# Performance work log

Hardware: AMD Instinct MI355X
Metric: run time of the kernel (lower is better)

Reference implementation:

```python
import jax, jax.numpy as jnp
import numpy as np

PI = np.pi


def _apply_1q(state, gate, wire, n):
    # state: [B, 2**n] complex64; gate: [2,2] (shared) or [B,2,2] (per-sample)
    # PennyLane convention: wire 0 is the most-significant bit of the state index.
    B = state.shape[0]
    left, right = 2 ** wire, 2 ** (n - wire - 1)
    s = state.reshape(B, left, 2, right)
    if gate.ndim == 2:
        s = jnp.einsum('kl,balr->bakr', gate, s)
    else:
        s = jnp.einsum('bkl,balr->bakr', gate, s)
    return s.reshape(B, -1)


def _apply_cz(state, wire, n):
    # CZ on (wire, wire+1): flip sign of |..11..> amplitudes
    B = state.shape[0]
    left, right = 2 ** wire, 2 ** (n - wire - 2)
    s = state.reshape(B, left, 2, 2, right)
    s = s.at[:, :, 1, 1, :].multiply(-1.0)
    return s.reshape(B, -1)


def _ry_batched(theta):
    # theta: [B] -> [B,2,2] complex RY(theta)
    h = 0.5 * theta
    c, s = jnp.cos(h), jnp.sin(h)
    g = jnp.stack([jnp.stack([c, -s], -1), jnp.stack([s, c], -1)], -2)
    return g.astype(jnp.complex64)


def _rot(phi, theta, omega):
    # Rot = RZ(omega) @ RY(theta) @ RZ(phi)
    c, s = jnp.cos(0.5 * theta), jnp.sin(0.5 * theta)
    e_mm = jnp.exp(-0.5j * (phi + omega))
    e_pm = jnp.exp(0.5j * (phi - omega))
    e_mp = jnp.exp(-0.5j * (phi - omega))
    e_pp = jnp.exp(0.5j * (phi + omega))
    g = jnp.stack([jnp.stack([e_mm * c, -e_pm * s]), jnp.stack([e_mp * s, e_pp * c])])
    return g.astype(jnp.complex64)


def _simulate(enc, weights):
    # enc: [B, n_qubits] in [-1,1]; weights: [n_layers, n_qubits, 3]
    n_layers, n, _ = weights.shape
    B = enc.shape[0]
    state = jnp.zeros((B, 2 ** n), jnp.complex64).at[:, 0].set(1.0)
    ry = [_ry_batched(enc[:, i] * PI) for i in range(n)]
    for l in range(n_layers):
        for i in range(n):
            state = _apply_1q(state, ry[i], i, n)
        for i in range(n):
            state = _apply_1q(state, _rot(weights[l, i, 0], weights[l, i, 1], weights[l, i, 2]), i, n)
        for i in range(n - 1):
            state = _apply_cz(state, i, n)
    for i in range(n):
        state = _apply_1q(state, ry[i], i, n)
    probs = state.real ** 2 + state.imag ** 2  # [B, 2**n]
    # <Z_i> = sum_k probs[k] * (-1)^bit_i(k), wire 0 = MSB
    bits = (jnp.arange(2 ** n)[None, :] >> (n - 1 - jnp.arange(n))[:, None]) & 1
    signs = (1 - 2 * bits).astype(probs.dtype)  # [n, 2**n]
    return probs @ signs.T  # [B, n]


def setup_inputs() -> dict:
    B, D, NQ, NL, NA = 32768, 16, 8, 4, 4
    key = jax.random.key(0)
    ks = jax.random.split(key, 6)

    def lin(k, o, i):
        b = 1.0 / np.sqrt(i)
        k1, k2 = jax.random.split(k)
        return (jax.random.uniform(k1, (o, i), jnp.float32, -b, b),
                jax.random.uniform(k2, (o,), jnp.float32, -b, b))

    enc_w1, enc_b1 = lin(ks[1], 8, D)
    enc_w2, enc_b2 = lin(ks[2], NQ, 8)
    dec_w1, dec_b1 = lin(ks[3], 8, NQ)
    dec_w2, dec_b2 = lin(ks[4], NA, 8)
    q_weights = jax.random.uniform(ks[5], (NL, NQ, 3), jnp.float32, 0.0, 2.0 * PI)
    x = jax.random.normal(ks[0], (B, D), jnp.float32)
    return {"x": x, "enc_w1": enc_w1, "enc_b1": enc_b1, "enc_w2": enc_w2, "enc_b2": enc_b2,
            "q_weights": q_weights, "dec_w1": dec_w1, "dec_b1": dec_b1, "dec_w2": dec_w2, "dec_b2": dec_b2}


def reference(x, enc_w1, enc_b1, enc_w2, enc_b2, q_weights, dec_w1, dec_b1, dec_w2, dec_b2):
    h = jax.nn.relu(x @ enc_w1.T + enc_b1)
    enc = jnp.tanh(h @ enc_w2.T + enc_b2)          # [B, n_qubits]
    q = _simulate(enc, q_weights)                  # [B, n_qubits] PauliZ expvals
    h2 = jax.nn.relu(q @ dec_w1.T + dec_b1)
    return h2 @ dec_w2.T + dec_b2                  # [B, n_actions]
```

## Files before the change

### kernel.cpp

```cpp
#include <hip/hip_runtime.h>
#include <math.h>


#define PI_F 3.14159265358979323846f

typedef float v2f __attribute__((ext_vector_type(2)));

struct C2 { float re, im; };
__device__ __forceinline__ C2 cmul(C2 a, C2 b) {
    C2 r;
    r.re = fmaf(a.re, b.re, -a.im * b.im);
    r.im = fmaf(a.re, b.im,  a.im * b.re);
    return r;
}
__device__ __forceinline__ float fxor(float x, int m) {
    return __int_as_float(__float_as_int(x) ^ m);
}

__device__ __forceinline__ v2f pk_mul(v2f a, v2f b) {
    v2f d; asm("v_pk_mul_f32 %0, %1, %2" : "=v"(d) : "v"(a), "v"(b)); return d;
}
__device__ __forceinline__ v2f pk_mul_neg(v2f a, v2f b) {
    v2f d; asm("v_pk_mul_f32 %0, %1, %2 neg_lo:[1,0] neg_hi:[1,0]"
               : "=v"(d) : "v"(a), "v"(b)); return d;
}
__device__ __forceinline__ v2f pk_fma(v2f a, v2f b, v2f c) {
    v2f d; asm("v_pk_fma_f32 %0, %1, %2, %3" : "=v"(d) : "v"(a), "v"(b), "v"(c)); return d;
}
__device__ __forceinline__ v2f pk_fma_nn(v2f a, v2f b, v2f c) {
    v2f d; asm("v_pk_fma_f32 %0, %1, %2, %3 neg_lo:[1,0,0] neg_hi:[1,0,0]"
               : "=v"(d) : "v"(a), "v"(b), "v"(c)); return d;
}
__device__ __forceinline__ v2f pk_fma_swl(v2f a, v2f b, v2f c) {
    v2f d; asm("v_pk_fma_f32 %0, %1, %2, %3 op_sel:[0,1,0] op_sel_hi:[1,0,1] neg_lo:[1,0,0]"
               : "=v"(d) : "v"(a), "v"(b), "v"(c)); return d;
}
__device__ __forceinline__ v2f pk_fma_swh(v2f a, v2f b, v2f c) {
    v2f d; asm("v_pk_fma_f32 %0, %1, %2, %3 op_sel:[0,1,0] op_sel_hi:[1,0,1] neg_hi:[1,0,0]"
               : "=v"(d) : "v"(a), "v"(b), "v"(c)); return d;
}

template<int CTRL>
__device__ __forceinline__ float dppf(float x) {
    int xi = __float_as_int(x);
    int r = __builtin_amdgcn_update_dpp(xi, xi, CTRL, 0xF, 0xF, false);
    return __int_as_float(r);
}
template<int M>
__device__ __forceinline__ float lxor(float x) {
    if constexpr (M == 1)      return dppf<0xB1>(x);
    else if constexpr (M == 2) return dppf<0x4E>(x);
    else if constexpr (M == 4) return __int_as_float(
        __builtin_amdgcn_ds_swizzle(__float_as_int(x), 0x101F));
    else                       return dppf<0x128>(x);
}

__device__ __forceinline__ void load_G2(const float* __restrict__ c_lds, int g,
                                        float cc, float ss,
                                        float& ar, float& ai, float& br, float& bi) {
    const float4 c0 = *(const float4*)(c_lds + 4 * g);
    ar = fmaf(c0.x, cc, -c0.z * ss);
    ai = fmaf(c0.y, cc,  c0.w * ss);
    br = fmaf(c0.z, cc,  c0.x * ss);
    bi = fmaf(c0.w, cc, -c0.y * ss);
}

template<int M>
__device__ __forceinline__ void su2_cross(v2f cSr, v2f cSi, v2f cOr, v2f cOi,
                                          v2f z[16]) {
#pragma unroll
    for (int t = 0; t < 16; t++) {
        v2f p;
        p.x = lxor<M>(z[t].x);
        p.y = lxor<M>(z[t].y);
        v2f n = pk_mul(cSr, z[t]);
        n = pk_fma_swl(cSi, z[t], n);
        n = pk_fma   (cOr, p, n);
        n = pk_fma_swl(cOi, p, n);
        z[t] = n;
    }
}

template<int ST>
__device__ __forceinline__ void su2_inlane(v2f arr, v2f aii, v2f brr, v2f bii,
                                           v2f z[16]) {
#pragma unroll
    for (int t = 0; t < 16; t++) {
        if ((t & ST) == 0) {
            const int u = t + ST;
            v2f x = z[t], y = z[u];
            v2f nx = pk_mul(arr, x);
            nx = pk_fma_swl(aii, x, nx);
            nx = pk_fma_nn (brr, y, nx);
            nx = pk_fma_swl(bii, y, nx);
            v2f ny = pk_mul(brr, x);
            ny = pk_fma_swl(bii, x, ny);
            ny = pk_fma   (arr, y, ny);
            ny = pk_fma_swh(aii, y, ny);
            z[t] = nx; z[u] = ny;
        }
    }
}

template<int M>
__device__ __forceinline__ void ry_cross(v2f cc, v2f cO, v2f z[16]) {
#pragma unroll
    for (int t = 0; t < 16; t++) {
        v2f p;
        p.x = lxor<M>(z[t].x);
        p.y = lxor<M>(z[t].y);
        z[t] = pk_fma(cO, p, pk_mul(cc, z[t]));
    }
}
template<int ST>
__device__ __forceinline__ void ry_inlane(v2f cc, v2f ss, v2f z[16]) {
#pragma unroll
    for (int t = 0; t < 16; t++) {
        if ((t & ST) == 0) {
            const int u = t + ST;
            v2f x = z[t], y = z[u];
            z[t] = pk_fma_nn(ss, y, pk_mul(cc, x));
            z[u] = pk_fma   (cc, y, pk_mul(ss, x));
        }
    }
}

__device__ __constant__ const bool CZNEG[16] =
    { false,false,false,true,  false,false,true,false,
      false,false,false,true,  true, true, false,true };

__global__ __launch_bounds__(256) void qdqn_kernel(
    const float* __restrict__ x,
    const float* __restrict__ ew1, const float* __restrict__ eb1,
    const float* __restrict__ ew2, const float* __restrict__ eb2,
    const float* __restrict__ qw,
    const float* __restrict__ dw1, const float* __restrict__ db1,
    const float* __restrict__ dw2, const float* __restrict__ db2,
    float* __restrict__ out, int B, int NL) {
    __shared__ __align__(16) float c_lds[32 * 4];

    const int tid = threadIdx.x;
    const int n_gates = NL * 8;

    if (tid < n_gates) {
        const int g = tid;
        float phi = qw[3 * g + 0], th = qw[3 * g + 1], om = qw[3 * g + 2];
        float c = __cosf(0.5f * th), s = __sinf(0.5f * th);
        float A = 0.5f * (phi + om), Bb = 0.5f * (phi - om);
        float* o = c_lds + 4 * g;
        o[0] =  __cosf(A) * c;  o[1] = -__sinf(A) * c;
        o[2] =  __cosf(Bb) * s; o[3] = -__sinf(Bb) * s;
    }
    __syncthreads();

    const int lane = tid & 63;
    const int L = lane & 15;
    int s = blockIdx.x * 16 + (tid >> 4);
    if (s >= B) s = B - 1;

    float xv[16];
    const float4* xp = (const float4*)(x + s * 16);
#pragma unroll
    for (int i = 0; i < 4; i++) {
        float4 v = xp[i];
        xv[4*i] = v.x; xv[4*i+1] = v.y; xv[4*i+2] = v.z; xv[4*i+3] = v.w;
    }
    float hbuf[8];
#pragma unroll
    for (int j = 0; j < 8; j++) {
        float a = eb1[j];
#pragma unroll
        for (int i = 0; i < 16; i++) a = fmaf(ew1[j * 16 + i], xv[i], a);
        hbuf[j] = fmaxf(a, 0.0f);
    }
    float cq[8], sq[8];
#pragma unroll
    for (int q = 0; q < 8; q++) {
        float a = eb2[q];
#pragma unroll
        for (int j = 0; j < 8; j++) a = fmaf(ew2[q * 8 + j], hbuf[j], a);
        float e = 1.0f - __fdividef(2.0f, __expf(2.0f * a) + 1.0f);
        float ang = e * (0.5f * PI_F);
        cq[q] = __cosf(ang);
        sq[q] = __sinf(ang);
    }

    int hiM[4], loM[4];
#pragma unroll
    for (int q = 0; q < 4; q++) {
        int hi = (L >> (3 - q)) & 1;
        hiM[q] = hi << 31;
        loM[q] = hiM[q] ^ 0x80000000;
    }

    const int L0 = L & 1, L1b = (L >> 1) & 1, L2b = (L >> 2) & 1, L3b = (L >> 3) & 1;
    const int cnt = (L3b & L2b) + (L2b & L1b) + (L1b & L0);
    const float mL = (cnt & 1) ? -1.0f : 1.0f;
    const float mH = L0 ? -mL : mL;
    const v2f mL2 = (v2f){mL, mL}, mH2 = (v2f){mH, mH};

    v2f z[16];
    {
        C2 P; P.re = 1.0f; P.im = 0.0f;
        C2 F[4][2];
#pragma unroll
        for (int q = 0; q < 8; q++) {
            float ar, ai, br, bi;
            load_G2(c_lds, q, cq[q], sq[q], ar, ai, br, bi);
            if (q < 4) {
                const bool hi = (L >> (3 - q)) & 1;
                C2 f; f.re = hi ? br : ar; f.im = hi ? bi : ai;
                P = cmul(P, f);
            } else {
                F[q-4][0].re = ar; F[q-4][0].im = ai;
                F[q-4][1].re = br; F[q-4][1].im = bi;
            }
        }
        C2 A0 = cmul(P, F[0][0]), A1 = cmul(P, F[0][1]);
        C2 Bv[4];
        Bv[0] = cmul(A0, F[1][0]); Bv[1] = cmul(A0, F[1][1]);
        Bv[2] = cmul(A1, F[1][0]); Bv[3] = cmul(A1, F[1][1]);
        C2 Cv[8];
#pragma unroll
        for (int i = 0; i < 8; i++) Cv[i] = cmul(Bv[i >> 1], F[2][i & 1]);
#pragma unroll
        for (int t = 0; t < 16; t++) {
            C2 v = cmul(Cv[t >> 1], F[3][t & 1]);
            float m = (t < 8) ? mL : mH;
            m = CZNEG[t] ? -m : m;
            z[t].x = v.re * m;
            z[t].y = v.im * m;
        }
    }

    for (int l = 1; l < NL; l++) {
        const int g0 = l * 8;
        float ar, ai, br, bi;
        load_G2(c_lds, g0+0, cq[0], sq[0], ar, ai, br, bi);
        su2_cross<8>((v2f){ar,ar}, (v2f){fxor(ai,hiM[0]),fxor(ai,hiM[0])},
                     (v2f){fxor(br,loM[0]),fxor(br,loM[0])}, (v2f){bi,bi}, z);
        load_G2(c_lds, g0+1, cq[1], sq[1], ar, ai, br, bi);
        su2_cross<4>((v2f){ar,ar}, (v2f){fxor(ai,hiM[1]),fxor(ai,hiM[1])},
                     (v2f){fxor(br,loM[1]),fxor(br,loM[1])}, (v2f){bi,bi}, z);
        load_G2(c_lds, g0+2, cq[2], sq[2], ar, ai, br, bi);
        su2_cross<2>((v2f){ar,ar}, (v2f){fxor(ai,hiM[2]),fxor(ai,hiM[2])},
                     (v2f){fxor(br,loM[2]),fxor(br,loM[2])}, (v2f){bi,bi}, z);
        load_G2(c_lds, g0+3, cq[3], sq[3], ar, ai, br, bi);
        su2_cross<1>((v2f){ar,ar}, (v2f){fxor(ai,hiM[3]),fxor(ai,hiM[3])},
                     (v2f){fxor(br,loM[3]),fxor(br,loM[3])}, (v2f){bi,bi}, z);
        load_G2(c_lds, g0+4, cq[4], sq[4], ar, ai, br, bi);
        su2_inlane<8>((v2f){ar,ar}, (v2f){ai,ai}, (v2f){br,br}, (v2f){bi,bi}, z);
        load_G2(c_lds, g0+5, cq[5], sq[5], ar, ai, br, bi);
        su2_inlane<4>((v2f){ar,ar}, (v2f){ai,ai}, (v2f){br,br}, (v2f){bi,bi}, z);
        load_G2(c_lds, g0+6, cq[6], sq[6], ar, ai, br, bi);
        su2_inlane<2>((v2f){ar,ar}, (v2f){ai,ai}, (v2f){br,br}, (v2f){bi,bi}, z);
        load_G2(c_lds, g0+7, cq[7], sq[7], ar, ai, br, bi);
        su2_inlane<1>((v2f){ar,ar}, (v2f){ai,ai}, (v2f){br,br}, (v2f){bi,bi}, z);
#pragma unroll
        for (int t = 0; t < 16; t++) {
            v2f m = (t < 8) ? mL2 : mH2;
            z[t] = CZNEG[t] ? pk_mul_neg(m, z[t]) : pk_mul(m, z[t]);
        }
    }

    {
        v2f cc, cO, ss;
        cc=(v2f){cq[0],cq[0]}; cO=(v2f){fxor(sq[0],loM[0]),fxor(sq[0],loM[0])};
        ry_cross<8>(cc, cO, z);
        cc=(v2f){cq[1],cq[1]}; cO=(v2f){fxor(sq[1],loM[1]),fxor(sq[1],loM[1])};
        ry_cross<4>(cc, cO, z);
        cc=(v2f){cq[2],cq[2]}; cO=(v2f){fxor(sq[2],loM[2]),fxor(sq[2],loM[2])};
        ry_cross<2>(cc, cO, z);
        cc=(v2f){cq[3],cq[3]}; cO=(v2f){fxor(sq[3],loM[3]),fxor(sq[3],loM[3])};
        ry_cross<1>(cc, cO, z);
        cc=(v2f){cq[4],cq[4]}; ss=(v2f){sq[4],sq[4]}; ry_inlane<8>(cc, ss, z);
        cc=(v2f){cq[5],cq[5]}; ss=(v2f){sq[5],sq[5]}; ry_inlane<4>(cc, ss, z);
        cc=(v2f){cq[6],cq[6]}; ss=(v2f){sq[6],sq[6]}; ry_inlane<2>(cc, ss, z);
        cc=(v2f){cq[7],cq[7]}; ss=(v2f){sq[7],sq[7]}; ry_inlane<1>(cc, ss, z);
    }

    float p[16];
#pragma unroll
    for (int t = 0; t < 16; t++) p[t] = fmaf(z[t].x, z[t].x, z[t].y * z[t].y);

    float e0 = p[0]+p[1],  e1 = p[2]+p[3],  e2 = p[4]+p[5],  e3 = p[6]+p[7];
    float e4 = p[8]+p[9],  e5 = p[10]+p[11], e6 = p[12]+p[13], e7 = p[14]+p[15];
    float q0 = e0+e1, q1 = e2+e3, q2 = e4+e5, q3 = e6+e7;
    float h0 = q0+q1, h1 = q2+q3;
    float sumP = h0 + h1;

    float zv[8];
#pragma unroll
    for (int w = 0; w < 4; w++)
        zv[w] = ((L >> (3 - w)) & 1) ? -sumP : sumP;
    zv[4] = h0 - h1;
    zv[5] = (q0 - q1) + (q2 - q3);
    zv[6] = (e0 - e1) + (e2 - e3) + (e4 - e5) + (e6 - e7);
    zv[7] = (p[0]-p[1]) + (p[2]-p[3]) + (p[4]-p[5]) + (p[6]-p[7])
          + (p[8]-p[9]) + (p[10]-p[11]) + (p[12]-p[13]) + (p[14]-p[15]);

#pragma unroll
    for (int w = 0; w < 8; w++) zv[w] += lxor<1>(zv[w]);
#pragma unroll
    for (int w = 0; w < 8; w++) zv[w] += lxor<2>(zv[w]);
#pragma unroll
    for (int w = 0; w < 8; w++) zv[w] += lxor<4>(zv[w]);
#pragma unroll
    for (int w = 0; w < 8; w++) zv[w] += lxor<8>(zv[w]);

    float h2[8];
#pragma unroll
    for (int j = 0; j < 8; j++) {
        float a = db1[j];
#pragma unroll
        for (int w = 0; w < 8; w++) a = fmaf(dw1[j * 8 + w], zv[w], a);
        h2[j] = fmaxf(a, 0.0f);
    }
    if (L < 4) {
        float a = db2[L];
#pragma unroll
        for (int j = 0; j < 8; j++) a = fmaf(dw2[L * 8 + j], h2[j], a);
        out[s * 4 + L] = a;
    }
}

extern "C" void kernel_launch(void* const* d_in, const int* in_sizes, int n_in,
                              void* d_out, int out_size, void* d_ws, size_t ws_size,
                              hipStream_t stream) {
    const float* x   = (const float*)d_in[0];
    const float* ew1 = (const float*)d_in[1];
    const float* eb1 = (const float*)d_in[2];
    const float* ew2 = (const float*)d_in[3];
    const float* eb2 = (const float*)d_in[4];
    const float* qw  = (const float*)d_in[5];
    const float* dw1 = (const float*)d_in[6];
    const float* db1 = (const float*)d_in[7];
    const float* dw2 = (const float*)d_in[8];
    const float* db2 = (const float*)d_in[9];
    float* out = (float*)d_out;

    int B = in_sizes[0] / 16;
    int n_gates = in_sizes[5] / 3;
    int NL = n_gates / 8;

    int blocks = (B + 15) / 16;
    qdqn_kernel<<<blocks, 256, 0, stream>>>(x, ew1, eb1, ew2, eb2, qw,
                                            dw1, db1, dw2, db2, out, B, NL);
}
```

Measured before the change: 124.1 us.

## Map each sample to 8 lanes with 32 amplitudes per lane

Each sample's 256-amplitude state now lives on 8 lanes holding 32 amplitudes each, where it used to be 16 lanes holding 16. The top three qubits are handled by cross-lane shuffles and the other five in-lane, and the block shrinks to 128 threads with launch bounds of 128,2. The encoder and decoder MLPs are also split across the 8 lanes, with results exchanged through LDS and wave barriers so each lane no longer computes every hidden unit. This cuts the cross-lane shuffle traffic and redundant MLP work, but the larger per-lane state raises register pressure and gives fewer threads per sample.

```diff
diff --git a/kernel.cpp b/kernel.cpp
--- a/kernel.cpp
+++ b/kernel.cpp
@@ -39,6 +39,10 @@
     v2f d; asm("v_pk_fma_f32 %0, %1, %2, %3 op_sel:[0,1,0] op_sel_hi:[1,0,1] neg_hi:[1,0,0]"
                : "=v"(d) : "v"(a), "v"(b), "v"(c)); return d;
 }
+__device__ __forceinline__ v2f cmulv(v2f z, C2 c) {
+    v2f n = pk_mul((v2f){c.re, c.re}, z);
+    return pk_fma_swl((v2f){c.im, c.im}, z, n);
+}
 
 template<int CTRL>
 __device__ __forceinline__ float dppf(float x) {
@@ -50,9 +54,8 @@
 __device__ __forceinline__ float lxor(float x) {
     if constexpr (M == 1)      return dppf<0xB1>(x);
     else if constexpr (M == 2) return dppf<0x4E>(x);
-    else if constexpr (M == 4) return __int_as_float(
+    else                       return __int_as_float(
         __builtin_amdgcn_ds_swizzle(__float_as_int(x), 0x101F));
-    else                       return dppf<0x128>(x);
 }
 
 __device__ __forceinline__ void load_G2(const float* __restrict__ c_lds, int g,
@@ -67,9 +70,9 @@
 
 template<int M>
 __device__ __forceinline__ void su2_cross(v2f cSr, v2f cSi, v2f cOr, v2f cOi,
-                                          v2f z[16]) {
-#pragma unroll
-    for (int t = 0; t < 16; t++) {
+                                          v2f z[32]) {
+#pragma unroll
+    for (int t = 0; t < 32; t++) {
         v2f p;
         p.x = lxor<M>(z[t].x);
         p.y = lxor<M>(z[t].y);
@@ -83,9 +86,9 @@
 
 template<int ST>
 __device__ __forceinline__ void su2_inlane(v2f arr, v2f aii, v2f brr, v2f bii,
-                                           v2f z[16]) {
-#pragma unroll
-    for (int t = 0; t < 16; t++) {
+                                           v2f z[32]) {
+#pragma unroll
+    for (int t = 0; t < 32; t++) {
         if ((t & ST) == 0) {
             const int u = t + ST;
             v2f x = z[t], y = z[u];
@@ -103,9 +106,9 @@
 }
 
 template<int M>
-__device__ __forceinline__ void ry_cross(v2f cc, v2f cO, v2f z[16]) {
-#pragma unroll
-    for (int t = 0; t < 16; t++) {
+__device__ __forceinline__ void ry_cross(v2f cc, v2f cO, v2f z[32]) {
+#pragma unroll
+    for (int t = 0; t < 32; t++) {
         v2f p;
         p.x = lxor<M>(z[t].x);
         p.y = lxor<M>(z[t].y);
@@ -113,9 +116,9 @@
     }
 }
 template<int ST>
-__device__ __forceinline__ void ry_inlane(v2f cc, v2f ss, v2f z[16]) {
-#pragma unroll
-    for (int t = 0; t < 16; t++) {
+__device__ __forceinline__ void ry_inlane(v2f cc, v2f ss, v2f z[32]) {
+#pragma unroll
+    for (int t = 0; t < 32; t++) {
         if ((t & ST) == 0) {
             const int u = t + ST;
             v2f x = z[t], y = z[u];
@@ -125,11 +128,12 @@
     }
 }
 
-__device__ __constant__ const bool CZNEG[16] =
-    { false,false,false,true,  false,false,true,false,
-      false,false,false,true,  true, true, false,true };
-
-__global__ __launch_bounds__(256) void qdqn_kernel(
+__host__ __device__ constexpr bool czt5(int t) {
+    return ((((t >> 4) & (t >> 3)) ^ ((t >> 3) & (t >> 2)) ^
+             ((t >> 2) & (t >> 1)) ^ ((t >> 1) & t)) & 1) != 0;
+}
+
+__global__ __launch_bounds__(128, 2) void qdqn_kernel(
     const float* __restrict__ x,
     const float* __restrict__ ew1, const float* __restrict__ eb1,
     const float* __restrict__ ew2, const float* __restrict__ eb2,
@@ -138,6 +142,8 @@
     const float* __restrict__ dw2, const float* __restrict__ db2,
     float* __restrict__ out, int B, int NL) {
     __shared__ __align__(16) float c_lds[32 * 4];
+    __shared__ __align__(16) float hx[2][8][8];
+    __shared__ __align__(16) float csx[2][8][16];
 
     const int tid = threadIdx.x;
     const int n_gates = NL * 8;
@@ -153,174 +159,195 @@
     }
     __syncthreads();
 
+    const int wave = tid >> 6;
     const int lane = tid & 63;
-    const int L = lane & 15;
-    int s = blockIdx.x * 16 + (tid >> 4);
+    const int grp = lane >> 3;
+    const int g = lane & 7;
+    int s = blockIdx.x * 16 + wave * 8 + grp;
     if (s >= B) s = B - 1;
 
-    float xv[16];
-    const float4* xp = (const float4*)(x + s * 16);
-#pragma unroll
-    for (int i = 0; i < 4; i++) {
-        float4 v = xp[i];
-        xv[4*i] = v.x; xv[4*i+1] = v.y; xv[4*i+2] = v.z; xv[4*i+3] = v.w;
-    }
-    float hbuf[8];
-#pragma unroll
-    for (int j = 0; j < 8; j++) {
-        float a = eb1[j];
-#pragma unroll
-        for (int i = 0; i < 16; i++) a = fmaf(ew1[j * 16 + i], xv[i], a);
-        hbuf[j] = fmaxf(a, 0.0f);
-    }
     float cq[8], sq[8];
-#pragma unroll
-    for (int q = 0; q < 8; q++) {
-        float a = eb2[q];
-#pragma unroll
-        for (int j = 0; j < 8; j++) a = fmaf(ew2[q * 8 + j], hbuf[j], a);
-        float e = 1.0f - __fdividef(2.0f, __expf(2.0f * a) + 1.0f);
+    {
+        float xv[16];
+        const float4* xp = (const float4*)(x + s * 16);
+#pragma unroll
+        for (int i = 0; i < 4; i++) {
+            float4 v = xp[i];
+            xv[4*i] = v.x; xv[4*i+1] = v.y; xv[4*i+2] = v.z; xv[4*i+3] = v.w;
+        }
+        float a = eb1[g];
+#pragma unroll
+        for (int i = 0; i < 16; i++) a = fmaf(ew1[g * 16 + i], xv[i], a);
+        hx[wave][grp][g] = fmaxf(a, 0.0f);
+        __builtin_amdgcn_wave_barrier();
+        float4 h01 = *(const float4*)&hx[wave][grp][0];
+        float4 h23 = *(const float4*)&hx[wave][grp][4];
+        float b = eb2[g];
+        b = fmaf(ew2[g*8+0], h01.x, b); b = fmaf(ew2[g*8+1], h01.y, b);
+        b = fmaf(ew2[g*8+2], h01.z, b); b = fmaf(ew2[g*8+3], h01.w, b);
+        b = fmaf(ew2[g*8+4], h23.x, b); b = fmaf(ew2[g*8+5], h23.y, b);
+        b = fmaf(ew2[g*8+6], h23.z, b); b = fmaf(ew2[g*8+7], h23.w, b);
+        float e = 1.0f - __fdividef(2.0f, __expf(2.0f * b) + 1.0f);
         float ang = e * (0.5f * PI_F);
-        cq[q] = __cosf(ang);
-        sq[q] = __sinf(ang);
-    }
-
-    int hiM[4], loM[4];
-#pragma unroll
-    for (int q = 0; q < 4; q++) {
-        int hi = (L >> (3 - q)) & 1;
+        float2* cso = (float2*)&csx[wave][grp][2 * g];
+        *cso = make_float2(__cosf(ang), __sinf(ang));
+        __builtin_amdgcn_wave_barrier();
+#pragma unroll
+        for (int k = 0; k < 4; k++) {
+            float4 v = *(const float4*)&csx[wave][grp][4 * k];
+            cq[2*k] = v.x; sq[2*k] = v.y; cq[2*k+1] = v.z; sq[2*k+1] = v.w;
+        }
+    }
+
+    int hiM[3], loM[3];
+#pragma unroll
+    for (int q = 0; q < 3; q++) {
+        int hi = (g >> (2 - q)) & 1;
         hiM[q] = hi << 31;
         loM[q] = hiM[q] ^ 0x80000000;
     }
 
-    const int L0 = L & 1, L1b = (L >> 1) & 1, L2b = (L >> 2) & 1, L3b = (L >> 3) & 1;
-    const int cnt = (L3b & L2b) + (L2b & L1b) + (L1b & L0);
-    const float mL = (cnt & 1) ? -1.0f : 1.0f;
-    const float mH = L0 ? -mL : mL;
-    const v2f mL2 = (v2f){mL, mL}, mH2 = (v2f){mH, mH};
-
-    v2f z[16];
+    const int g0b = g & 1, g1b = (g >> 1) & 1, g2b = (g >> 2) & 1;
+    const float mLo = ((g2b & g1b) ^ (g1b & g0b)) ? -1.0f : 1.0f;
+    const float mHi = g0b ? -mLo : mLo;
+    const v2f mLo2 = (v2f){mLo, mLo}, mHi2 = (v2f){mHi, mHi};
+
+    v2f z[32];
     {
         C2 P; P.re = 1.0f; P.im = 0.0f;
-        C2 F[4][2];
+        C2 A[5], Bc[5];
 #pragma unroll
         for (int q = 0; q < 8; q++) {
             float ar, ai, br, bi;
             load_G2(c_lds, q, cq[q], sq[q], ar, ai, br, bi);
-            if (q < 4) {
-                const bool hi = (L >> (3 - q)) & 1;
+            if (q < 3) {
+                const bool hi = (g >> (2 - q)) & 1;
                 C2 f; f.re = hi ? br : ar; f.im = hi ? bi : ai;
                 P = cmul(P, f);
             } else {
-                F[q-4][0].re = ar; F[q-4][0].im = ai;
-                F[q-4][1].re = br; F[q-4][1].im = bi;
+                A[q-3].re = ar;  A[q-3].im = ai;
+                Bc[q-3].re = br; Bc[q-3].im = bi;
             }
         }
-        C2 A0 = cmul(P, F[0][0]), A1 = cmul(P, F[0][1]);
-        C2 Bv[4];
-        Bv[0] = cmul(A0, F[1][0]); Bv[1] = cmul(A0, F[1][1]);
-        Bv[2] = cmul(A1, F[1][0]); Bv[3] = cmul(A1, F[1][1]);
-        C2 Cv[8];
-#pragma unroll
-        for (int i = 0; i < 8; i++) Cv[i] = cmul(Bv[i >> 1], F[2][i & 1]);
-#pragma unroll
-        for (int t = 0; t < 16; t++) {
-            C2 v = cmul(Cv[t >> 1], F[3][t & 1]);
-            float m = (t < 8) ? mL : mH;
-            m = CZNEG[t] ? -m : m;
-            z[t].x = v.re * m;
-            z[t].y = v.im * m;
+        z[0] = (v2f){P.re, P.im};
+#pragma unroll
+        for (int w = 0; w < 5; w++) {
+            const int n = 1 << w;
+#pragma unroll
+            for (int i = n - 1; i >= 0; i--) {
+                v2f v = z[i];
+                z[2*i+1] = cmulv(v, Bc[w]);
+                z[2*i]   = cmulv(v, A[w]);
+            }
+        }
+#pragma unroll
+        for (int t = 0; t < 32; t++) {
+            v2f m = (t < 16) ? mLo2 : mHi2;
+            z[t] = czt5(t) ? pk_mul_neg(m, z[t]) : pk_mul(m, z[t]);
         }
     }
 
     for (int l = 1; l < NL; l++) {
-        const int g0 = l * 8;
+        const int gb = l * 8;
         float ar, ai, br, bi;
-        load_G2(c_lds, g0+0, cq[0], sq[0], ar, ai, br, bi);
-        su2_cross<8>((v2f){ar,ar}, (v2f){fxor(ai,hiM[0]),fxor(ai,hiM[0])},
+        load_G2(c_lds, gb+0, cq[0], sq[0], ar, ai, br, bi);
+        su2_cross<4>((v2f){ar,ar}, (v2f){fxor(ai,hiM[0]),fxor(ai,hiM[0])},
                      (v2f){fxor(br,loM[0]),fxor(br,loM[0])}, (v2f){bi,bi}, z);
-        load_G2(c_lds, g0+1, cq[1], sq[1], ar, ai, br, bi);
-        su2_cross<4>((v2f){ar,ar}, (v2f){fxor(ai,hiM[1]),fxor(ai,hiM[1])},
+        load_G2(c_lds, gb+1, cq[1], sq[1], ar, ai, br, bi);
+        su2_cross<2>((v2f){ar,ar}, (v2f){fxor(ai,hiM[1]),fxor(ai,hiM[1])},
                      (v2f){fxor(br,loM[1]),fxor(br,loM[1])}, (v2f){bi,bi}, z);
-        load_G2(c_lds, g0+2, cq[2], sq[2], ar, ai, br, bi);
-        su2_cross<2>((v2f){ar,ar}, (v2f){fxor(ai,hiM[2]),fxor(ai,hiM[2])},
+        load_G2(c_lds, gb+2, cq[2], sq[2], ar, ai, br, bi);
+        su2_cross<1>((v2f){ar,ar}, (v2f){fxor(ai,hiM[2]),fxor(ai,hiM[2])},
                      (v2f){fxor(br,loM[2]),fxor(br,loM[2])}, (v2f){bi,bi}, z);
-        load_G2(c_lds, g0+3, cq[3], sq[3], ar, ai, br, bi);
-        su2_cross<1>((v2f){ar,ar}, (v2f){fxor(ai,hiM[3]),fxor(ai,hiM[3])},
-                     (v2f){fxor(br,loM[3]),fxor(br,loM[3])}, (v2f){bi,bi}, z);
-        load_G2(c_lds, g0+4, cq[4], sq[4], ar, ai, br, bi);
+        load_G2(c_lds, gb+3, cq[3], sq[3], ar, ai, br, bi);
+        su2_inlane<16>((v2f){ar,ar}, (v2f){ai,ai}, (v2f){br,br}, (v2f){bi,bi}, z);
+        load_G2(c_lds, gb+4, cq[4], sq[4], ar, ai, br, bi);
         su2_inlane<8>((v2f){ar,ar}, (v2f){ai,ai}, (v2f){br,br}, (v2f){bi,bi}, z);
-        load_G2(c_lds, g0+5, cq[5], sq[5], ar, ai, br, bi);
+        load_G2(c_lds, gb+5, cq[5], sq[5], ar, ai, br, bi);
         su2_inlane<4>((v2f){ar,ar}, (v2f){ai,ai}, (v2f){br,br}, (v2f){bi,bi}, z);
-        load_G2(c_lds, g0+6, cq[6], sq[6], ar, ai, br, bi);
+        load_G2(c_lds, gb+6, cq[6], sq[6], ar, ai, br, bi);
         su2_inlane<2>((v2f){ar,ar}, (v2f){ai,ai}, (v2f){br,br}, (v2f){bi,bi}, z);
-        load_G2(c_lds, g0+7, cq[7], sq[7], ar, ai, br, bi);
+        load_G2(c_lds, gb+7, cq[7], sq[7], ar, ai, br, bi);
         su2_inlane<1>((v2f){ar,ar}, (v2f){ai,ai}, (v2f){br,br}, (v2f){bi,bi}, z);
 #pragma unroll
-        for (int t = 0; t < 16; t++) {
-            v2f m = (t < 8) ? mL2 : mH2;
-            z[t] = CZNEG[t] ? pk_mul_neg(m, z[t]) : pk_mul(m, z[t]);
+        for (int t = 0; t < 32; t++) {
+            v2f m = (t < 16) ? mLo2 : mHi2;
+            z[t] = czt5(t) ? pk_mul_neg(m, z[t]) : pk_mul(m, z[t]);
         }
     }
 
     {
         v2f cc, cO, ss;
         cc=(v2f){cq[0],cq[0]}; cO=(v2f){fxor(sq[0],loM[0]),fxor(sq[0],loM[0])};
-        ry_cross<8>(cc, cO, z);
+        ry_cross<4>(cc, cO, z);
         cc=(v2f){cq[1],cq[1]}; cO=(v2f){fxor(sq[1],loM[1]),fxor(sq[1],loM[1])};
-        ry_cross<4>(cc, cO, z);
+        ry_cross<2>(cc, cO, z);
         cc=(v2f){cq[2],cq[2]}; cO=(v2f){fxor(sq[2],loM[2]),fxor(sq[2],loM[2])};
-        ry_cross<2>(cc, cO, z);
-        cc=(v2f){cq[3],cq[3]}; cO=(v2f){fxor(sq[3],loM[3]),fxor(sq[3],loM[3])};
         ry_cross<1>(cc, cO, z);
+        cc=(v2f){cq[3],cq[3]}; ss=(v2f){sq[3],sq[3]}; ry_inlane<16>(cc, ss, z);
         cc=(v2f){cq[4],cq[4]}; ss=(v2f){sq[4],sq[4]}; ry_inlane<8>(cc, ss, z);
         cc=(v2f){cq[5],cq[5]}; ss=(v2f){sq[5],sq[5]}; ry_inlane<4>(cc, ss, z);
         cc=(v2f){cq[6],cq[6]}; ss=(v2f){sq[6],sq[6]}; ry_inlane<2>(cc, ss, z);
         cc=(v2f){cq[7],cq[7]}; ss=(v2f){sq[7],sq[7]}; ry_inlane<1>(cc, ss, z);
     }
 
-    float p[16];
-#pragma unroll
-    for (int t = 0; t < 16; t++) p[t] = fmaf(z[t].x, z[t].x, z[t].y * z[t].y);
-
-    float e0 = p[0]+p[1],  e1 = p[2]+p[3],  e2 = p[4]+p[5],  e3 = p[6]+p[7];
-    float e4 = p[8]+p[9],  e5 = p[10]+p[11], e6 = p[12]+p[13], e7 = p[14]+p[15];
-    float q0 = e0+e1, q1 = e2+e3, q2 = e4+e5, q3 = e6+e7;
-    float h0 = q0+q1, h1 = q2+q3;
-    float sumP = h0 + h1;
-
-    float zv[8];
-#pragma unroll
-    for (int w = 0; w < 4; w++)
-        zv[w] = ((L >> (3 - w)) & 1) ? -sumP : sumP;
-    zv[4] = h0 - h1;
-    zv[5] = (q0 - q1) + (q2 - q3);
-    zv[6] = (e0 - e1) + (e2 - e3) + (e4 - e5) + (e6 - e7);
-    zv[7] = (p[0]-p[1]) + (p[2]-p[3]) + (p[4]-p[5]) + (p[6]-p[7])
-          + (p[8]-p[9]) + (p[10]-p[11]) + (p[12]-p[13]) + (p[14]-p[15]);
-
-#pragma unroll
-    for (int w = 0; w < 8; w++) zv[w] += lxor<1>(zv[w]);
-#pragma unroll
-    for (int w = 0; w < 8; w++) zv[w] += lxor<2>(zv[w]);
-#pragma unroll
-    for (int w = 0; w < 8; w++) zv[w] += lxor<4>(zv[w]);
-#pragma unroll
-    for (int w = 0; w < 8; w++) zv[w] += lxor<8>(zv[w]);
-
-    float h2[8];
-#pragma unroll
-    for (int j = 0; j < 8; j++) {
-        float a = db1[j];
-#pragma unroll
-        for (int w = 0; w < 8; w++) a = fmaf(dw1[j * 8 + w], zv[w], a);
-        h2[j] = fmaxf(a, 0.0f);
-    }
-    if (L < 4) {
-        float a = db2[L];
-#pragma unroll
-        for (int j = 0; j < 8; j++) a = fmaf(dw2[L * 8 + j], h2[j], a);
-        out[s * 4 + L] = a;
+    float p[32];
+#pragma unroll
+    for (int t = 0; t < 32; t++) p[t] = fmaf(z[t].x, z[t].x, z[t].y * z[t].y);
+
+    float s16[16], zW[8];
+    {
+        float d = 0.0f;
+#pragma unroll
+        for (int i = 0; i < 16; i++) {
+            s16[i] = p[2*i] + p[2*i+1];
+            d += p[2*i] - p[2*i+1];
+        }
+        zW[7] = d;
+        float s8[8]; d = 0.0f;
+#pragma unroll
+        for (int i = 0; i < 8; i++) {
+            s8[i] = s16[2*i] + s16[2*i+1];
+            d += s16[2*i] - s16[2*i+1];
+        }
+        zW[6] = d;
+        float s4[4]; d = 0.0f;
+#pragma unroll
+        for (int i = 0; i < 4; i++) {
+            s4[i] = s8[2*i] + s8[2*i+1];
+            d += s8[2*i] - s8[2*i+1];
+        }
+        zW[5] = d;
+        float s2a = s4[0] + s4[1], s2b = s4[2] + s4[3];
+        zW[4] = (s4[0] - s4[1]) + (s4[2] - s4[3]);
+        float sumP = s2a + s2b;
+        zW[3] = s2a - s2b;
+        zW[0] = g2b ? -sumP : sumP;
+        zW[1] = g1b ? -sumP : sumP;
+        zW[2] = g0b ? -sumP : sumP;
+    }
+#pragma unroll
+    for (int w = 0; w < 8; w++) zW[w] += lxor<1>(zW[w]);
+#pragma unroll
+    for (int w = 0; w < 8; w++) zW[w] += lxor<2>(zW[w]);
+#pragma unroll
+    for (int w = 0; w < 8; w++) zW[w] += lxor<4>(zW[w]);
+
+    {
+        float a = db1[g];
+#pragma unroll
+        for (int w = 0; w < 8; w++) a = fmaf(dw1[g * 8 + w], zW[w], a);
+        hx[wave][grp][g] = fmaxf(a, 0.0f);
+        __builtin_amdgcn_wave_barrier();
+        float4 h01 = *(const float4*)&hx[wave][grp][0];
+        float4 h23 = *(const float4*)&hx[wave][grp][4];
+        const int o = g & 3;
+        float acc = db2[o];
+        acc = fmaf(dw2[o*8+0], h01.x, acc); acc = fmaf(dw2[o*8+1], h01.y, acc);
+        acc = fmaf(dw2[o*8+2], h01.z, acc); acc = fmaf(dw2[o*8+3], h01.w, acc);
+        acc = fmaf(dw2[o*8+4], h23.x, acc); acc = fmaf(dw2[o*8+5], h23.y, acc);
+        acc = fmaf(dw2[o*8+6], h23.z, acc); acc = fmaf(dw2[o*8+7], h23.w, acc);
+        out[s * 4 + o] = acc;
     }
 }
 
@@ -344,6 +371,6 @@
     int NL = n_gates / 8;
 
     int blocks = (B + 15) / 16;
-    qdqn_kernel<<<blocks, 256, 0, stream>>>(x, ew1, eb1, ew2, eb2, qw,
+    qdqn_kernel<<<blocks, 128, 0, stream>>>(x, ew1, eb1, ew2, eb2, qw,
                                             dw1, db1, dw2, db2, out, B, NL);
 }
```

Result: faster. 119.8 us (-3.5%).
